# Kernel tuning notes

Hardware: AMD Instinct MI355X
Metric: run time of the kernel (lower is better)

The kernel has to match this reference:

```python
import jax, jax.numpy as jnp
import numpy as np
import math

B, N, T, D, H, NOUT = 32, 20, 100, 4, 128, 16
E = N * (N - 1)
EPS = 1e-5

def _conv1d(x, w, b):
    # x: [M, Cin, L], w: [Cout, Cin, K] -> [M, Cout, L-K+1] (VALID, stride 1)
    y = jax.lax.conv_general_dilated(x, w, (1,), 'VALID', dimension_numbers=('NCH', 'OIH', 'NCH'))
    return y + b[None, :, None]

def _bn(x, g, b, axes, caxis):
    # training-mode batch norm (biased variance), eps as in torch
    m = jnp.mean(x, axis=axes, keepdims=True)
    v = jnp.var(x, axis=axes, keepdims=True)
    sh = [1] * x.ndim
    sh[caxis] = -1
    return (x - m) / jnp.sqrt(v + EPS) * g.reshape(sh) + b.reshape(sh)

def _mlp(x, w1, b1, w2, b2, g, bb):
    h = jax.nn.elu(x @ w1.T + b1)
    h = jax.nn.elu(h @ w2.T + b2)
    return _bn(h, g, bb, (0, 1), 2)  # BN over B*E samples per feature

def _forward(rel_rec, rel_send, inputs, conv1_w, conv1_b, bn1_g, bn1_b, conv2_w, conv2_b, bn2_g, bn2_b, pred_w, pred_b, att_w, att_b, mlp1_w1, mlp1_b1, mlp1_w2, mlp1_b2, mlp1_g, mlp1_bb, mlp2_w1, mlp2_b1, mlp2_w2, mlp2_b2, mlp2_g, mlp2_bb, mlp3_w1, mlp3_b1, mlp3_w2, mlp3_b2, mlp3_g, mlp3_bb, fc_out_w, fc_out_b):
    Bv, Nv, Tv, Dv = inputs.shape
    Ev = Nv * (Nv - 1)
    # node2edge_temporal: gather sender/receiver trajectories -> [B*E, 2D, T]
    xf = inputs.reshape(Bv, Nv, Tv * Dv)
    recv = jnp.einsum('en,bnf->bef', rel_rec, xf).reshape(Bv * Ev, Tv, Dv).transpose(0, 2, 1)
    send = jnp.einsum('en,bnf->bef', rel_send, xf).reshape(Bv * Ev, Tv, Dv).transpose(0, 2, 1)
    edges = jnp.concatenate([send, recv], axis=1)
    # CNN over time
    h = jax.nn.relu(_conv1d(edges, conv1_w, conv1_b))
    h = _bn(h, bn1_g, bn1_b, (0, 2), 1)
    L = h.shape[-1] // 2
    h = h[:, :, : 2 * L].reshape(h.shape[0], h.shape[1], L, 2).max(axis=-1)  # maxpool k=2 s=2
    h = jax.nn.relu(_conv1d(h, conv2_w, conv2_b))
    h = _bn(h, bn2_g, bn2_b, (0, 2), 1)
    pred = jnp.einsum('bct,oc->bot', h, pred_w[:, :, 0]) + pred_b[None, :, None]
    att = jax.nn.softmax(jnp.einsum('bct,oc->bot', h, att_w[:, :, 0]) + att_b[None, :, None], axis=-1)
    x = (pred * att).mean(axis=-1).reshape(Bv, Ev, -1)  # attention-weighted mean pool
    x = _mlp(x, mlp1_w1, mlp1_b1, mlp1_w2, mlp1_b2, mlp1_g, mlp1_bb)
    x_skip = x
    # edge2node: scatter-mean into receivers (divide by N)
    xn = jnp.einsum('en,beh->bnh', rel_rec, x) / Nv
    xn = _mlp(xn, mlp2_w1, mlp2_b1, mlp2_w2, mlp2_b2, mlp2_g, mlp2_bb)
    # node2edge: gather back to edges
    es = jnp.einsum('en,bnh->beh', rel_send, xn)
    er = jnp.einsum('en,bnh->beh', rel_rec, xn)
    x = jnp.concatenate([es, er, x_skip], axis=2)
    x = _mlp(x, mlp3_w1, mlp3_b1, mlp3_w2, mlp3_b2, mlp3_g, mlp3_bb)
    return x @ fc_out_w.T + fc_out_b

def setup_inputs() -> dict:
    key = jax.random.key(0)
    ks = iter(jax.random.split(key, 64))
    def rn(shape, scale):
        return jax.random.normal(next(ks), shape, dtype=jnp.float32) * scale
    def xav(fo, fi):
        return rn((fo, fi), math.sqrt(2.0 / (fo + fi)))
    inputs = rn((B, N, T, D), 1.0)
    pairs = np.array([(i, j) for i in range(N) for j in range(N) if i != j])
    eye = np.eye(N, dtype=np.float32)
    d = {'inputs': inputs,
         'rel_rec': jnp.asarray(eye[pairs[:, 0]]),
         'rel_send': jnp.asarray(eye[pairs[:, 1]])}
    d['conv1_w'] = rn((H, 2 * D, 5), math.sqrt(2.0 / (5 * H)))
    d['conv1_b'] = jnp.full((H,), 0.1, jnp.float32)
    d['bn1_g'] = jnp.ones((H,), jnp.float32); d['bn1_b'] = jnp.zeros((H,), jnp.float32)
    d['conv2_w'] = rn((H, H, 5), math.sqrt(2.0 / (5 * H)))
    d['conv2_b'] = jnp.full((H,), 0.1, jnp.float32)
    d['bn2_g'] = jnp.ones((H,), jnp.float32); d['bn2_b'] = jnp.zeros((H,), jnp.float32)
    d['pred_w'] = rn((H, H, 1), math.sqrt(2.0 / H))
    d['pred_b'] = jnp.full((H,), 0.1, jnp.float32)
    d['att_w'] = rn((1, H, 1), math.sqrt(2.0))
    d['att_b'] = jnp.full((1,), 0.1, jnp.float32)
    for nm, fi in (('mlp1', H), ('mlp2', H), ('mlp3', 3 * H)):
        d[nm + '_w1'] = xav(H, fi); d[nm + '_b1'] = jnp.full((H,), 0.1, jnp.float32)
        d[nm + '_w2'] = xav(H, H); d[nm + '_b2'] = jnp.full((H,), 0.1, jnp.float32)
        d[nm + '_g'] = jnp.ones((H,), jnp.float32); d[nm + '_bb'] = jnp.zeros((H,), jnp.float32)
    d['fc_out_w'] = xav(NOUT, H)
    d['fc_out_b'] = jnp.full((NOUT,), 0.1, jnp.float32)
    return d

def reference(inputs, rel_rec, rel_send, conv1_w, conv1_b, bn1_g, bn1_b, conv2_w, conv2_b, bn2_g, bn2_b, pred_w, pred_b, att_w, att_b, mlp1_w1, mlp1_b1, mlp1_w2, mlp1_b2, mlp1_g, mlp1_bb, mlp2_w1, mlp2_b1, mlp2_w2, mlp2_b2, mlp2_g, mlp2_bb, mlp3_w1, mlp3_b1, mlp3_w2, mlp3_b2, mlp3_g, mlp3_bb, fc_out_w, fc_out_b):
    return _forward(rel_rec, rel_send, inputs, conv1_w, conv1_b, bn1_g, bn1_b, conv2_w, conv2_b, bn2_g, bn2_b, pred_w, pred_b, att_w, att_b, mlp1_w1, mlp1_b1, mlp1_w2, mlp1_b2, mlp1_g, mlp1_bb, mlp2_w1, mlp2_b1, mlp2_w2, mlp2_b2, mlp2_g, mlp2_bb, mlp3_w1, mlp3_b1, mlp3_w2, mlp3_b2, mlp3_g, mlp3_bb, fc_out_w, fc_out_b)
```

## Files before the change

kernel.cpp:

```cpp
#include <hip/hip_runtime.h>
#include <hip/hip_bf16.h>
#include <hip/hip_fp16.h>

#define BB 32
#define NN 20
#define TT 100
#define DD 4
#define HH 128
#define EE 380
#define BE 12160
#define L1 96
#define LP 48
#define L2 44
#define NOUT 16
#define EPS 1e-5f
#define NREP 64

typedef _Float16 f16x8 __attribute__((ext_vector_type(8)));
typedef _Float16 f16x4 __attribute__((ext_vector_type(4)));
typedef _Float16 f16x2 __attribute__((ext_vector_type(2)));
typedef float f32x4 __attribute__((ext_vector_type(4)));

#define S_BIAS2 0
#define S_BN1_SC 256
#define S_BN2_SC 768
#define S_M1_SC 1280
#define S_M2_SC 1792
#define S_M3_SC 2304

#define OFF_STATS 0ULL
#define OFF_SIDX 16384ULL
#define OFF_RIDX 18432ULL
#define OFF_INC 20480ULL
#define OFF_Y23 24576ULL
#define OFF_X 149446656ULL
#define OFF_BUFA 155672576ULL
#define OFF_BUFB 161898496ULL
#define OFF_XN 168124416ULL
#define OFF_T640 168452096ULL
#define OFF_REPM 168779776ULL
#define OFF_MP 171958272ULL
#define OFF_APACK OFF_T640
#define OFF_APACK1 (OFF_T640 + 163840ULL)
#define OFF_PWT (OFF_T640 + 180224ULL)
#define OFF_W2SUM (OFF_T640 + 245760ULL)
#define OFF_REP1 OFF_BUFA
#define OFF_REP2 (OFF_BUFA + 65536ULL)
#define MP_M1W1 0
#define MP_M1W2 16384
#define MP_M2W1 32768
#define MP_M2W2 49152
#define MP_M3W2 65536
#define MP_M3W1 81920

__device__ __forceinline__ float eluf(float v) { return v > 0.f ? v : expm1f(v); }

__global__ __launch_bounds__(256) void k_prep(const float* __restrict__ rel_rec,
                                              const float* __restrict__ rel_send,
                                              const float* __restrict__ w2,
                                              const float* __restrict__ w1,
                                              const float* __restrict__ pred_w,
                                              const float* __restrict__ m1w1,
                                              const float* __restrict__ m1w2,
                                              const float* __restrict__ m2w1,
                                              const float* __restrict__ m2w2,
                                              const float* __restrict__ m3w1,
                                              const float* __restrict__ m3w2,
                                              _Float16* __restrict__ apack,
                                              _Float16* __restrict__ apack1,
                                              float* __restrict__ pwt,
                                              float* __restrict__ w2sum,
                                              _Float16* __restrict__ mp,
                                              float* rep1, float* rep2, float* repm,
                                              int* sidx, int* ridx, int* inc) {
    int b = blockIdx.x;
    int tid = threadIdx.x;
    int l = tid & 63;
    if (b < 40) {
        int f = b * 4 + (tid >> 6);
        int m0 = f & 7, ks = f >> 3, s = ks & 3, k = ks >> 2;
        int m = m0 * 16 + (l & 15);
        int cbase = 32 * s + (l >> 4) * 8;
#pragma unroll
        for (int j = 0; j < 8; ++j)
            apack[(f * 64 + l) * 8 + j] = (_Float16)w2[m * 640 + (cbase + j) * 5 + k];
    } else if (b < 44) {
        int f = (b - 40) * 4 + (tid >> 6);
        int m0 = f & 7, s = f >> 3;
        int m = m0 * 16 + (l & 15);
        int cbase = 32 * s + (l >> 4) * 8;
#pragma unroll
        for (int j = 0; j < 8; ++j) {
            int c = cbase + j;
            int k = c >> 3, ci = c & 7;
            apack1[(f * 64 + l) * 8 + j] = (k < 5) ? (_Float16)w1[m * 40 + ci * 5 + k]
                                                   : (_Float16)0.f;
        }
    } else if (b == 44) {
        for (int i = tid; i < NREP * 256; i += 256) { rep1[i] = 0.f; rep2[i] = 0.f; repm[i] = 0.f; }
        for (int e = tid; e < EE; e += 256) {
            int s = 0, r = 0;
            for (int n = 0; n < NN; ++n) {
                if (rel_send[e * NN + n] > 0.5f) s = n;
                if (rel_rec[e * NN + n] > 0.5f) r = n;
            }
            sidx[e] = s; ridx[e] = r;
        }
        __syncthreads();
        if (tid < NN) {
            int k = 0;
            for (int e = 0; e < EE; ++e)
                if (ridx[e] == tid) inc[tid * (NN - 1) + (k++)] = e;
        }
    } else if (b < 53) {
        int idx = (b - 45) * 2048 + tid;
        for (int rep = 0; rep < 8; ++rep, idx += 256) {
            int o = idx >> 7, c = idx & 127;
            pwt[c * 128 + o] = pred_w[idx];
        }
    } else if (b < 117) {
        int idx = b - 53;
        const float* W; _Float16* dst; int K;
        if (idx < 8)       { W = m1w1; dst = mp + MP_M1W1; K = 128; }
        else if (idx < 16) { W = m1w2; dst = mp + MP_M1W2; K = 128; idx -= 8; }
        else if (idx < 24) { W = m2w1; dst = mp + MP_M2W1; K = 128; idx -= 16; }
        else if (idx < 32) { W = m2w2; dst = mp + MP_M2W2; K = 128; idx -= 24; }
        else if (idx < 40) { W = m3w2; dst = mp + MP_M3W2; K = 128; idx -= 32; }
        else               { W = m3w1; dst = mp + MP_M3W1; K = 384; idx -= 40; }
        int f = idx * 4 + (tid >> 6);
        int s = f >> 3, m0 = f & 7;
        int m = m0 * 16 + (l & 15);
        int cb = 32 * s + (l >> 4) * 8;
#pragma unroll
        for (int j = 0; j < 8; ++j)
            dst[(f * 64 + l) * 8 + j] = (_Float16)W[m * K + cb + j];
    } else {
        int idx = (b - 117) * 2048 + tid;
        for (int rep = 0; rep < 8; ++rep, idx += 256) {
            const float* wr = w2 + idx * 5;
            w2sum[idx] = wr[0] + wr[1] + wr[2] + wr[3] + wr[4];
        }
    }
}

__global__ __launch_bounds__(256) void k_conv1_stats(const float* __restrict__ inputs,
                                                     const _Float16* __restrict__ apack1,
                                                     const float* __restrict__ conv1_b,
                                                     const int* __restrict__ sidx,
                                                     const int* __restrict__ ridx,
                                                     float* rep1,
                                                     _Float16* __restrict__ y2p) {
    __shared__ __align__(16) _Float16 s_edgesT[104 * 8];
    __shared__ __align__(16) _Float16 s_y2t[48 * 136];
    int be = blockIdx.x;
    int b = be / EE, e = be - b * EE;
    int sn = sidx[e], rn = ridx[e];
    float* rep = rep1 + (be & (NREP - 1)) * 256;
    for (int i = threadIdx.x; i < 200; i += 256) {
        int side = (i >= 100) ? 1 : 0;
        int t = i - side * 100;
        int n = side ? rn : sn;
        float4 v = *(const float4*)(inputs + ((long long)(b * NN + n) * TT + t) * DD);
        f16x4 o = {(_Float16)v.x, (_Float16)v.y, (_Float16)v.z, (_Float16)v.w};
        *(f16x4*)(&s_edgesT[t * 8 + side * 4]) = o;
    }
    if (threadIdx.x < 32) s_edgesT[800 + threadIdx.x] = (_Float16)0.f;
    __syncthreads();
    int w = threadIdx.x >> 6, lane = threadIdx.x & 63;
    int quad = lane >> 4, l15 = lane & 15;
    f32x4 acc1[2][6];
#pragma unroll
    for (int m = 0; m < 2; ++m)
#pragma unroll
        for (int nt = 0; nt < 6; ++nt) acc1[m][nt] = (f32x4){0.f, 0.f, 0.f, 0.f};
    {
        const f16x8* Ap = (const f16x8*)apack1;
#pragma unroll
        for (int s = 0; s < 2; ++s) {
            f16x8 a0 = Ap[(s * 8 + 2 * w) * 64 + lane];
            f16x8 a1 = Ap[(s * 8 + 2 * w + 1) * 64 + lane];
#pragma unroll
            for (int nt = 0; nt < 6; ++nt) {
                f16x8 bfr = *(const f16x8*)(&s_edgesT[(nt * 16 + l15 + 4 * s + quad) * 8]);
                acc1[0][nt] = __builtin_amdgcn_mfma_f32_16x16x32_f16(a0, bfr, acc1[0][nt], 0, 0, 0);
                acc1[1][nt] = __builtin_amdgcn_mfma_f32_16x16x32_f16(a1, bfr, acc1[1][nt], 0, 0, 0);
            }
        }
    }
#pragma unroll
    for (int m = 0; m < 2; ++m) {
        int co0 = (2 * w + m) * 16 + quad * 4;
        float ss[4] = {0.f, 0.f, 0.f, 0.f}, qq[4] = {0.f, 0.f, 0.f, 0.f};
#pragma unroll
        for (int nt = 0; nt < 6; ++nt) {
            int t = nt * 16 + l15;
#pragma unroll
            for (int r = 0; r < 4; ++r) {
                float v = fmaxf(acc1[m][nt][r] + conv1_b[co0 + r], 0.f);
                ss[r] += v; qq[r] += v * v;
                float p = __shfl_xor(v, 1);
                if ((l15 & 1) == 0)
                    s_y2t[(t >> 1) * 136 + co0 + r] = (_Float16)fmaxf(v, p);
            }
        }
#pragma unroll
        for (int r = 0; r < 4; ++r) {
            float s = ss[r], q = qq[r];
            s += __shfl_xor(s, 1); s += __shfl_xor(s, 2); s += __shfl_xor(s, 4); s += __shfl_xor(s, 8);
            q += __shfl_xor(q, 1); q += __shfl_xor(q, 2); q += __shfl_xor(q, 4); q += __shfl_xor(q, 8);
            if (l15 == 0) {
                atomicAdd(&rep[co0 + r], s);
                atomicAdd(&rep[128 + co0 + r], q);
            }
        }
    }
    __syncthreads();
    _Float16* dst = y2p + (long long)be * 6144;
    for (int chunk = threadIdx.x; chunk < 768; chunk += 256) {
        int row = chunk >> 4, off = (chunk & 15) * 8;
        *(f16x8*)(dst + row * 128 + off) = *(const f16x8*)(&s_y2t[row * 136 + off]);
    }
}

__global__ void k_finalize_rep(float* __restrict__ rep, float* stats, int scIdx,
                               const float* __restrict__ g, const float* __restrict__ bb,
                               float inv_count) {
    int j = threadIdx.x;
    float s = 0.f, q = 0.f;
    for (int i = 0; i < NREP; ++i) {
        s += rep[i * 256 + j];
        q += rep[i * 256 + 128 + j];
    }
    for (int i = 0; i < NREP; ++i) {
        rep[i * 256 + j] = 0.f;
        rep[i * 256 + 128 + j] = 0.f;
    }
    float m = s * inv_count;
    float v = fmaxf(q * inv_count - m * m, 0.f);
    float sc = g[j] * rsqrtf(v + EPS);
    stats[scIdx + j] = sc;
    stats[scIdx + 128 + j] = bb[j] - m * sc;
}

__global__ void k_finalize_bn1(float* __restrict__ rep, float* stats,
                               const float* __restrict__ g, const float* __restrict__ bb,
                               const float* __restrict__ w2sum, const float* __restrict__ conv2_b,
                               float inv_count) {
    __shared__ float s_sh[128];
    int j = threadIdx.x;
    float s = 0.f, q = 0.f;
    for (int i = 0; i < NREP; ++i) {
        s += rep[i * 256 + j];
        q += rep[i * 256 + 128 + j];
    }
    for (int i = 0; i < NREP; ++i) {
        rep[i * 256 + j] = 0.f;
        rep[i * 256 + 128 + j] = 0.f;
    }
    float m = s * inv_count;
    float v = fmaxf(q * inv_count - m * m, 0.f);
    float sc = g[j] * rsqrtf(v + EPS);
    float sh = bb[j] - m * sc;
    stats[S_BN1_SC + j] = sc;
    stats[S_BN1_SC + 128 + j] = sh;
    s_sh[j] = sh;
    __syncthreads();
    float acc = conv2_b[j];
    for (int ci = 0; ci < 128; ++ci)
        acc = fmaf(w2sum[j * 128 + ci], s_sh[ci], acc);
    stats[S_BIAS2 + j] = acc;
}

__global__ __launch_bounds__(256) void k_scale(_Float16* __restrict__ apack,
                                               const float* __restrict__ stats) {
    int tid = threadIdx.x, l = tid & 63;
    int f = blockIdx.x * 4 + (tid >> 6);
    int s = (f >> 3) & 3;
    int cbase = 32 * s + (l >> 4) * 8;
    _Float16* p = apack + (f * 64 + l) * 8;
#pragma unroll
    for (int j = 0; j < 8; ++j)
        p[j] = (_Float16)((float)p[j] * stats[S_BN1_SC + cbase + j]);
}

__global__ __launch_bounds__(256) void k_conv2(_Float16* __restrict__ y23,
                                               const _Float16* __restrict__ apack,
                                               const float* __restrict__ stats,
                                               float* rep2) {
    __shared__ __align__(16) _Float16 s_y2t[2][52 * 136];
    int tid = threadIdx.x;
    int be0 = blockIdx.x * 2;
    for (int i = tid; i < 544; i += 256) {
        int ed = i / 272, rem = i - ed * 272;
        ((int*)(&s_y2t[ed][48 * 136]))[rem] = 0;
    }
    for (int i = tid; i < 1536; i += 256) {
        int ed = i / 768, rem = i - ed * 768;
        int row = rem >> 4, c0 = (rem & 15) * 8;
        *(f16x8*)(&s_y2t[ed][row * 136 + c0]) =
            *(const f16x8*)(y23 + (long long)(be0 + ed) * 6144 + rem * 8);
    }
    __syncthreads();
    int w = tid >> 6, lane = tid & 63;
    int quad = lane >> 4, l15 = lane & 15;
    int g = w & 1, e = w >> 1;
    f32x4 acc[4][3];
#pragma unroll
    for (int m = 0; m < 4; ++m)
#pragma unroll
        for (int nt = 0; nt < 3; ++nt) acc[m][nt] = (f32x4){0.f, 0.f, 0.f, 0.f};
    const f16x8* Ap = (const f16x8*)apack;
    const char* base = (const char*)&s_y2t[e][0];
#pragma unroll
    for (int k = 0; k < 5; ++k) {
#pragma unroll
        for (int s = 0; s < 4; ++s) {
            f16x8 am[4];
#pragma unroll
            for (int m = 0; m < 4; ++m)
                am[m] = Ap[((k * 4 + s) * 8 + g * 4 + m) * 64 + lane];
#pragma unroll
            for (int nt = 0; nt < 3; ++nt) {
                f16x8 bfr = *(const f16x8*)(base + (nt * 16 + l15 + k) * 272 + 64 * s + quad * 16);
#pragma unroll
                for (int m = 0; m < 4; ++m)
                    acc[m][nt] = __builtin_amdgcn_mfma_f32_16x16x32_f16(am[m], bfr, acc[m][nt], 0, 0, 0);
            }
        }
    }
    int be = be0 + e;
    _Float16* y3 = y23 + (long long)be * 6144;
    float* rep = rep2 + (be & (NREP - 1)) * 256;
#pragma unroll
    for (int m = 0; m < 4; ++m) {
        int co0 = (g * 4 + m) * 16 + quad * 4;
        float4 bs = *(const float4*)(stats + S_BIAS2 + co0);
        float ssum[4] = {0.f, 0.f, 0.f, 0.f}, qsum[4] = {0.f, 0.f, 0.f, 0.f};
#pragma unroll
        for (int nt = 0; nt < 3; ++nt) {
            int t = nt * 16 + l15;
            if (t < 44) {
                float v0 = fmaxf(acc[m][nt][0] + bs.x, 0.f);
                float v1 = fmaxf(acc[m][nt][1] + bs.y, 0.f);
                float v2 = fmaxf(acc[m][nt][2] + bs.z, 0.f);
                float v3 = fmaxf(acc[m][nt][3] + bs.w, 0.f);
                f16x4 o = {(_Float16)v0, (_Float16)v1, (_Float16)v2, (_Float16)v3};
                *(f16x4*)(y3 + t * 128 + co0) = o;
                ssum[0] += v0; qsum[0] += v0 * v0;
                ssum[1] += v1; qsum[1] += v1 * v1;
                ssum[2] += v2; qsum[2] += v2 * v2;
                ssum[3] += v3; qsum[3] += v3 * v3;
            }
        }
#pragma unroll
        for (int r = 0; r < 4; ++r) {
            float s = ssum[r], q = qsum[r];
            s += __shfl_xor(s, 1); s += __shfl_xor(s, 2); s += __shfl_xor(s, 4); s += __shfl_xor(s, 8);
            q += __shfl_xor(q, 1); q += __shfl_xor(q, 2); q += __shfl_xor(q, 4); q += __shfl_xor(q, 8);
            if (l15 == 0) {
                atomicAdd(&rep[co0 + r], s);
                atomicAdd(&rep[128 + co0 + r], q);
            }
        }
    }
}

__global__ __launch_bounds__(256) void k_predatt(const _Float16* __restrict__ y23,
                                                 const float* __restrict__ stats,
                                                 const float* __restrict__ att_w,
                                                 const float* __restrict__ att_b,
                                                 const float* __restrict__ pwt,
                                                 const float* __restrict__ pred_b,
                                                 float* __restrict__ x) {
    __shared__ float h[44 * 132];
    __shared__ float s_att[48];
    __shared__ float s_p1[256];
    __shared__ float s_p2[256];
    __shared__ float s_sc[128], s_sh[128];
    int be = blockIdx.x, tid = threadIdx.x;
    if (tid < 128) {
        s_sc[tid] = stats[S_BN2_SC + tid];
        s_sh[tid] = stats[S_BN2_SC + 128 + tid];
    }
    __syncthreads();
    const _Float16* yp = y23 + (long long)be * 6144;
    for (int i = tid; i < 704; i += 256) {
        int t = i >> 4, c0 = (i & 15) * 8;
        f16x8 v = *(const f16x8*)(yp + i * 8);
        float4 a, bq;
        a.x = fmaf((float)v[0], s_sc[c0 + 0], s_sh[c0 + 0]);
        a.y = fmaf((float)v[1], s_sc[c0 + 1], s_sh[c0 + 1]);
        a.z = fmaf((float)v[2], s_sc[c0 + 2], s_sh[c0 + 2]);
        a.w = fmaf((float)v[3], s_sc[c0 + 3], s_sh[c0 + 3]);
        bq.x = fmaf((float)v[4], s_sc[c0 + 4], s_sh[c0 + 4]);
        bq.y = fmaf((float)v[5], s_sc[c0 + 5], s_sh[c0 + 5]);
        bq.z = fmaf((float)v[6], s_sc[c0 + 6], s_sh[c0 + 6]);
        bq.w = fmaf((float)v[7], s_sc[c0 + 7], s_sh[c0 + 7]);
        *(float4*)(&h[t * 132 + c0]) = a;
        *(float4*)(&h[t * 132 + c0 + 4]) = bq;
    }
    __syncthreads();
    int w = tid >> 6, lane = tid & 63;
    {
        float aw0 = att_w[lane], aw1 = att_w[64 + lane];
        for (int tt = 0; tt < 11; ++tt) {
            int t = w * 11 + tt;
            float p = h[t * 132 + lane] * aw0 + h[t * 132 + 64 + lane] * aw1;
            p += __shfl_xor(p, 1); p += __shfl_xor(p, 2); p += __shfl_xor(p, 4);
            p += __shfl_xor(p, 8); p += __shfl_xor(p, 16); p += __shfl_xor(p, 32);
            if (lane == 0) s_att[t] = p + att_b[0];
        }
    }
    __syncthreads();
    if (w == 0) {
        float v = (lane < 44) ? s_att[lane] : -1e30f;
        float m = v;
        m = fmaxf(m, __shfl_xor(m, 1)); m = fmaxf(m, __shfl_xor(m, 2));
        m = fmaxf(m, __shfl_xor(m, 4)); m = fmaxf(m, __shfl_xor(m, 8));
        m = fmaxf(m, __shfl_xor(m, 16)); m = fmaxf(m, __shfl_xor(m, 32));
        float ev = (lane < 44) ? expf(v - m) : 0.f;
        float ss = ev;
        ss += __shfl_xor(ss, 1); ss += __shfl_xor(ss, 2); ss += __shfl_xor(ss, 4);
        ss += __shfl_xor(ss, 8); ss += __shfl_xor(ss, 16); ss += __shfl_xor(ss, 32);
        if (lane < 44) s_att[lane] = ev / ss;
    }
    __syncthreads();
    {
        int c = tid & 127, hh = tid >> 7;
        float a = 0.f;
        for (int t = hh * 22; t < hh * 22 + 22; ++t) a = fmaf(h[t * 132 + c], s_att[t], a);
        s_p1[tid] = a;
    }
    __syncthreads();
    {
        int o = tid & 127, hh = tid >> 7;
        float a = 0.f;
        for (int c = hh * 64; c < hh * 64 + 64; ++c) {
            float hw = s_p1[c] + s_p1[128 + c];
            a = fmaf(pwt[c * 128 + o], hw, a);
        }
        s_p2[tid] = a;
    }
    __syncthreads();
    if (tid < 128) {
        float a = s_p2[tid] + s_p2[128 + tid] + pred_b[tid];
        x[(long long)be * 128 + tid] = a * (1.0f / 44.0f);
    }
}

__global__ __launch_bounds__(256) void k_mlp2x(const float* __restrict__ in,
                                               const _Float16* __restrict__ wp1,
                                               const float* __restrict__ b1,
                                               const _Float16* __restrict__ wp2,
                                               const float* __restrict__ b2,
                                               float* __restrict__ out,
                                               float* __restrict__ repm) {
    __shared__ __align__(16) _Float16 s_in[64 * 136];
    __shared__ __align__(16) _Float16 s_mid[64 * 136];
    int tid = threadIdx.x;
    long long r0 = (long long)blockIdx.x * 64;
    {
        const float4* src = (const float4*)(in + r0 * 128);
        for (int i = tid; i < 2048; i += 256) {
            int row = i >> 5, c0 = (i & 31) * 4;
            float4 v = src[i];
            f16x4 o = {(_Float16)v.x, (_Float16)v.y, (_Float16)v.z, (_Float16)v.w};
            *(f16x4*)(&s_in[row * 136 + c0]) = o;
        }
    }
    __syncthreads();
    int w = tid >> 6, lane = tid & 63, quad = lane >> 4, l15 = lane & 15;
    {
        f32x4 acc[2][4];
#pragma unroll
        for (int m = 0; m < 2; ++m)
#pragma unroll
            for (int nt = 0; nt < 4; ++nt) acc[m][nt] = (f32x4){0.f, 0.f, 0.f, 0.f};
        const f16x8* Ap = (const f16x8*)wp1;
#pragma unroll
        for (int s = 0; s < 4; ++s) {
            f16x8 a0 = Ap[(s * 8 + 2 * w) * 64 + lane];
            f16x8 a1 = Ap[(s * 8 + 2 * w + 1) * 64 + lane];
#pragma unroll
            for (int nt = 0; nt < 4; ++nt) {
                f16x8 bfr = *(const f16x8*)((const char*)s_in + (nt * 16 + l15) * 272 + 64 * s + quad * 16);
                acc[0][nt] = __builtin_amdgcn_mfma_f32_16x16x32_f16(a0, bfr, acc[0][nt], 0, 0, 0);
                acc[1][nt] = __builtin_amdgcn_mfma_f32_16x16x32_f16(a1, bfr, acc[1][nt], 0, 0, 0);
            }
        }
#pragma unroll
        for (int m = 0; m < 2; ++m) {
            int j0 = (2 * w + m) * 16 + quad * 4;
            float4 bs = *(const float4*)(b1 + j0);
#pragma unroll
            for (int nt = 0; nt < 4; ++nt) {
                int row = nt * 16 + l15;
                f16x4 o = {(_Float16)eluf(acc[m][nt][0] + bs.x),
                           (_Float16)eluf(acc[m][nt][1] + bs.y),
                           (_Float16)eluf(acc[m][nt][2] + bs.z),
                           (_Float16)eluf(acc[m][nt][3] + bs.w)};
                *(f16x4*)(&s_mid[row * 136 + j0]) = o;
            }
        }
    }
    __syncthreads();
    {
        f32x4 acc[2][4];
#pragma unroll
        for (int m = 0; m < 2; ++m)
#pragma unroll
            for (int nt = 0; nt < 4; ++nt) acc[m][nt] = (f32x4){0.f, 0.f, 0.f, 0.f};
        const f16x8* Ap = (const f16x8*)wp2;
#pragma unroll
        for (int s = 0; s < 4; ++s) {
            f16x8 a0 = Ap[(s * 8 + 2 * w) * 64 + lane];
            f16x8 a1 = Ap[(s * 8 + 2 * w + 1) * 64 + lane];
#pragma unroll
            for (int nt = 0; nt < 4; ++nt) {
                f16x8 bfr = *(const f16x8*)((const char*)s_mid + (nt * 16 + l15) * 272 + 64 * s + quad * 16);
                acc[0][nt] = __builtin_amdgcn_mfma_f32_16x16x32_f16(a0, bfr, acc[0][nt], 0, 0, 0);
                acc[1][nt] = __builtin_amdgcn_mfma_f32_16x16x32_f16(a1, bfr, acc[1][nt], 0, 0, 0);
            }
        }
#pragma unroll
        for (int m = 0; m < 2; ++m) {
            int j0 = (2 * w + m) * 16 + quad * 4;
            float4 bs = *(const float4*)(b2 + j0);
            float ss[4] = {0.f, 0.f, 0.f, 0.f}, qq[4] = {0.f, 0.f, 0.f, 0.f};
#pragma unroll
            for (int nt = 0; nt < 4; ++nt) {
                int row = nt * 16 + l15;
                float v0 = eluf(acc[m][nt][0] + bs.x);
                float v1 = eluf(acc[m][nt][1] + bs.y);
                float v2 = eluf(acc[m][nt][2] + bs.z);
                float v3 = eluf(acc[m][nt][3] + bs.w);
                float4 o = {v0, v1, v2, v3};
                *(float4*)(out + (r0 + row) * 128 + j0) = o;
                ss[0] += v0; qq[0] += v0 * v0;
                ss[1] += v1; qq[1] += v1 * v1;
                ss[2] += v2; qq[2] += v2 * v2;
                ss[3] += v3; qq[3] += v3 * v3;
            }
            float* rep = repm + (blockIdx.x & (NREP - 1)) * 256;
#pragma unroll
            for (int r = 0; r < 4; ++r) {
                float s = ss[r], q = qq[r];
                s += __shfl_xor(s, 1); s += __shfl_xor(s, 2); s += __shfl_xor(s, 4); s += __shfl_xor(s, 8);
                q += __shfl_xor(q, 1); q += __shfl_xor(q, 2); q += __shfl_xor(q, 4); q += __shfl_xor(q, 8);
                if (l15 == 0) {
                    atomicAdd(&rep[j0 + r], s);
                    atomicAdd(&rep[128 + j0 + r], q);
                }
            }
        }
    }
}

__global__ __launch_bounds__(256) void k_mlp3x(const float* __restrict__ xn,
                                               const float* __restrict__ bufB,
                                               const int* __restrict__ sidx,
                                               const int* __restrict__ ridx,
                                               const float* __restrict__ stats,
                                               const _Float16* __restrict__ wp1,
                                               const float* __restrict__ b1,
                                               const _Float16* __restrict__ wp2,
                                               const float* __restrict__ b2,
                                               float* __restrict__ out,
                                               float* __restrict__ repm) {
    __shared__ __align__(16) _Float16 s_b[64 * 392];
    __shared__ __align__(16) _Float16 s_mid[64 * 136];
    __shared__ float s_st[4][128];
    __shared__ int s_s[64], s_r[64];
    int tid = threadIdx.x;
    long long r0 = (long long)blockIdx.x * 64;
    if (tid < 128) {
        s_st[0][tid] = stats[S_M2_SC + tid];
        s_st[1][tid] = stats[S_M2_SC + 128 + tid];
        s_st[2][tid] = stats[S_M1_SC + tid];
        s_st[3][tid] = stats[S_M1_SC + 128 + tid];
    }
    if (tid < 64) {
        int r = (int)r0 + tid, b = r / EE, ed = r - b * EE;
        s_s[tid] = (b * NN + sidx[ed]) * 128;
        s_r[tid] = (b * NN + ridx[ed]) * 128;
    }
    __syncthreads();
    for (int i = tid; i < 8192; i += 256) {
        int row = i >> 7, j = i & 127;
        float sc2 = s_st[0][j], sh2 = s_st[1][j];
        s_b[row * 392 + j] = (_Float16)fmaf(xn[s_s[row] + j], sc2, sh2);
        s_b[row * 392 + 128 + j] = (_Float16)fmaf(xn[s_r[row] + j], sc2, sh2);
        s_b[row * 392 + 256 + j] = (_Float16)fmaf(bufB[(r0 + row) * 128 + j], s_st[2][j], s_st[3][j]);
    }
    __syncthreads();
    int w = tid >> 6, lane = tid & 63, quad = lane >> 4, l15 = lane & 15;
    {
        f32x4 acc[2][4];
#pragma unroll
        for (int m = 0; m < 2; ++m)
#pragma unroll
            for (int nt = 0; nt < 4; ++nt) acc[m][nt] = (f32x4){0.f, 0.f, 0.f, 0.f};
        const f16x8* Ap = (const f16x8*)wp1;
#pragma unroll
        for (int s = 0; s < 12; ++s) {
            f16x8 a0 = Ap[(s * 8 + 2 * w) * 64 + lane];
            f16x8 a1 = Ap[(s * 8 + 2 * w + 1) * 64 + lane];
#pragma unroll
            for (int nt = 0; nt < 4; ++nt) {
                f16x8 bfr = *(const f16x8*)((const char*)s_b + (nt * 16 + l15) * 784 + 64 * s + quad * 16);
                acc[0][nt] = __builtin_amdgcn_mfma_f32_16x16x32_f16(a0, bfr, acc[0][nt], 0, 0, 0);
                acc[1][nt] = __builtin_amdgcn_mfma_f32_16x16x32_f16(a1, bfr, acc[1][nt], 0, 0, 0);
            }
        }
#pragma unroll
        for (int m = 0; m < 2; ++m) {
            int j0 = (2 * w + m) * 16 + quad * 4;
            float4 bs = *(const float4*)(b1 + j0);
#pragma unroll
            for (int nt = 0; nt < 4; ++nt) {
                int row = nt * 16 + l15;
                f16x4 o = {(_Float16)eluf(acc[m][nt][0] + bs.x),
                           (_Float16)eluf(acc[m][nt][1] + bs.y),
                           (_Float16)eluf(acc[m][nt][2] + bs.z),
                           (_Float16)eluf(acc[m][nt][3] + bs.w)};
                *(f16x4*)(&s_mid[row * 136 + j0]) = o;
            }
        }
    }
    __syncthreads();
    {
        f32x4 acc[2][4];
#pragma unroll
        for (int m = 0; m < 2; ++m)
#pragma unroll
            for (int nt = 0; nt < 4; ++nt) acc[m][nt] = (f32x4){0.f, 0.f, 0.f, 0.f};
        const f16x8* Ap = (const f16x8*)wp2;
#pragma unroll
        for (int s = 0; s < 4; ++s) {
            f16x8 a0 = Ap[(s * 8 + 2 * w) * 64 + lane];
            f16x8 a1 = Ap[(s * 8 + 2 * w + 1) * 64 + lane];
#pragma unroll
            for (int nt = 0; nt < 4; ++nt) {
                f16x8 bfr = *(const f16x8*)((const char*)s_mid + (nt * 16 + l15) * 272 + 64 * s + quad * 16);
                acc[0][nt] = __builtin_amdgcn_mfma_f32_16x16x32_f16(a0, bfr, acc[0][nt], 0, 0, 0);
                acc[1][nt] = __builtin_amdgcn_mfma_f32_16x16x32_f16(a1, bfr, acc[1][nt], 0, 0, 0);
            }
        }
#pragma unroll
        for (int m = 0; m < 2; ++m) {
            int j0 = (2 * w + m) * 16 + quad * 4;
            float4 bs = *(const float4*)(b2 + j0);
            float ss[4] = {0.f, 0.f, 0.f, 0.f}, qq[4] = {0.f, 0.f, 0.f, 0.f};
#pragma unroll
            for (int nt = 0; nt < 4; ++nt) {
                int row = nt * 16 + l15;
                float v0 = eluf(acc[m][nt][0] + bs.x);
                float v1 = eluf(acc[m][nt][1] + bs.y);
                float v2 = eluf(acc[m][nt][2] + bs.z);
                float v3 = eluf(acc[m][nt][3] + bs.w);
                float4 o = {v0, v1, v2, v3};
                *(float4*)(out + (r0 + row) * 128 + j0) = o;
                ss[0] += v0; qq[0] += v0 * v0;
                ss[1] += v1; qq[1] += v1 * v1;
                ss[2] += v2; qq[2] += v2 * v2;
                ss[3] += v3; qq[3] += v3 * v3;
            }
            float* rep = repm + (blockIdx.x & (NREP - 1)) * 256;
#pragma unroll
            for (int r = 0; r < 4; ++r) {
                float s = ss[r], q = qq[r];
                s += __shfl_xor(s, 1); s += __shfl_xor(s, 2); s += __shfl_xor(s, 4); s += __shfl_xor(s, 8);
                q += __shfl_xor(q, 1); q += __shfl_xor(q, 2); q += __shfl_xor(q, 4); q += __shfl_xor(q, 8);
                if (l15 == 0) {
                    atomicAdd(&rep[j0 + r], s);
                    atomicAdd(&rep[128 + j0 + r], q);
                }
            }
        }
    }
}

__global__ __launch_bounds__(128) void k_e2n(const float* __restrict__ bufB,
                                             const int* __restrict__ inc,
                                             const float* __restrict__ stats,
                                             float* __restrict__ xn) {
    int bn = blockIdx.x;
    int b = bn / NN, n = bn - b * NN;
    int j = threadIdx.x;
    float sc = stats[S_M1_SC + j], sh = stats[S_M1_SC + 128 + j];
    float s = 0.f;
    for (int k = 0; k < NN - 1; ++k) {
        int e = inc[n * (NN - 1) + k];
        s += bufB[(long long)(b * EE + e) * 128 + j];
    }
    xn[bn * 128 + j] = (s * sc + (float)(NN - 1) * sh) * (1.0f / (float)NN);
}

__global__ __launch_bounds__(256) void k_fcout(const float* __restrict__ h2,
                                               const float* __restrict__ stats,
                                               const float* __restrict__ fcw,
                                               const float* __restrict__ fcb,
                                               float* __restrict__ out) {
    __shared__ float s_x[16 * 129];
    __shared__ float s_w[16 * 129];
    int r0 = blockIdx.x * 16;
    int tid = threadIdx.x;
    for (int i = tid; i < 16 * 128; i += 256) {
        int rr = i >> 7, j = i & 127;
        s_x[rr * 129 + j] = fmaf(h2[(long long)(r0 + rr) * 128 + j],
                                 stats[S_M3_SC + j], stats[S_M3_SC + 128 + j]);
    }
    for (int i = tid; i < 16 * 128; i += 256) {
        int o = i >> 7, j = i & 127;
        s_w[o * 129 + j] = fcw[i];
    }
    __syncthreads();
    int rl = tid >> 4, o = tid & 15;
    float a = fcb[o];
    for (int j = 0; j < 128; ++j) a = fmaf(s_x[rl * 129 + j], s_w[o * 129 + j], a);
    out[(long long)(r0 + rl) * 16 + o] = a;
}

extern "C" void kernel_launch(void* const* d_in, const int* in_sizes, int n_in,
                              void* d_out, int out_size, void* d_ws, size_t ws_size,
                              hipStream_t stream) {
    const float* inputs = (const float*)d_in[0];
    const float* rel_rec = (const float*)d_in[1];
    const float* rel_send = (const float*)d_in[2];
    const float* conv1_w = (const float*)d_in[3];
    const float* conv1_b = (const float*)d_in[4];
    const float* bn1_g = (const float*)d_in[5];
    const float* bn1_b = (const float*)d_in[6];
    const float* conv2_w = (const float*)d_in[7];
    const float* conv2_b = (const float*)d_in[8];
    const float* bn2_g = (const float*)d_in[9];
    const float* bn2_b = (const float*)d_in[10];
    const float* pred_w = (const float*)d_in[11];
    const float* pred_b = (const float*)d_in[12];
    const float* att_w = (const float*)d_in[13];
    const float* att_b = (const float*)d_in[14];
    const float* m1w1 = (const float*)d_in[15];
    const float* m1b1 = (const float*)d_in[16];
    const float* m1w2 = (const float*)d_in[17];
    const float* m1b2 = (const float*)d_in[18];
    const float* m1g = (const float*)d_in[19];
    const float* m1bb = (const float*)d_in[20];
    const float* m2w1 = (const float*)d_in[21];
    const float* m2b1 = (const float*)d_in[22];
    const float* m2w2 = (const float*)d_in[23];
    const float* m2b2 = (const float*)d_in[24];
    const float* m2g = (const float*)d_in[25];
    const float* m2bb = (const float*)d_in[26];
    const float* m3w1 = (const float*)d_in[27];
    const float* m3b1 = (const float*)d_in[28];
    const float* m3w2 = (const float*)d_in[29];
    const float* m3b2 = (const float*)d_in[30];
    const float* m3g = (const float*)d_in[31];
    const float* m3bb = (const float*)d_in[32];
    const float* fcw = (const float*)d_in[33];
    const float* fcb = (const float*)d_in[34];

    char* ws = (char*)d_ws;
    float* stats = (float*)(ws + OFF_STATS);
    int* sidx = (int*)(ws + OFF_SIDX);
    int* ridx = (int*)(ws + OFF_RIDX);
    int* inc = (int*)(ws + OFF_INC);
    _Float16* y23 = (_Float16*)(ws + OFF_Y23);
    float* x = (float*)(ws + OFF_X);
    float* bufB = (float*)(ws + OFF_BUFB);
    float* xn = (float*)(ws + OFF_XN);
    _Float16* apack = (_Float16*)(ws + OFF_APACK);
    _Float16* apack1 = (_Float16*)(ws + OFF_APACK1);
    float* pwt = (float*)(ws + OFF_PWT);
    float* w2sum = (float*)(ws + OFF_W2SUM);
    float* rep1 = (float*)(ws + OFF_REP1);
    float* rep2 = (float*)(ws + OFF_REP2);
    float* repm = (float*)(ws + OFF_REPM);
    _Float16* mp = (_Float16*)(ws + OFF_MP);
    float* outp = (float*)d_out;

    hipLaunchKernelGGL(k_prep, dim3(125), dim3(256), 0, stream,
                       rel_rec, rel_send, conv2_w, conv1_w, pred_w,
                       m1w1, m1w2, m2w1, m2w2, m3w1, m3w2,
                       apack, apack1, pwt, w2sum, mp, rep1, rep2, repm, sidx, ridx, inc);
    hipLaunchKernelGGL(k_conv1_stats, dim3(BE), dim3(256), 0, stream,
                       inputs, apack1, conv1_b, sidx, ridx, rep1, y23);
    hipLaunchKernelGGL(k_finalize_bn1, dim3(1), dim3(128), 0, stream,
                       rep1, stats, bn1_g, bn1_b, w2sum, conv2_b, 1.0f / (float)(BE * L1));
    hipLaunchKernelGGL(k_scale, dim3(40), dim3(256), 0, stream, apack, stats);
    hipLaunchKernelGGL(k_conv2, dim3(BE / 2), dim3(256), 0, stream,
                       y23, apack, stats, rep2);
    hipLaunchKernelGGL(k_finalize_rep, dim3(1), dim3(128), 0, stream,
                       rep2, stats, S_BN2_SC, bn2_g, bn2_b, 1.0f / (float)(BE * L2));
    hipLaunchKernelGGL(k_predatt, dim3(BE), dim3(256), 0, stream,
                       y23, stats, att_w, att_b, pwt, pred_b, x);
    hipLaunchKernelGGL(k_mlp2x, dim3(BE / 64), dim3(256), 0, stream,
                       x, mp + MP_M1W1, m1b1, mp + MP_M1W2, m1b2, bufB, repm);
    hipLaunchKernelGGL(k_finalize_rep, dim3(1), dim3(128), 0, stream,
                       repm, stats, S_M1_SC, m1g, m1bb, 1.0f / (float)BE);
    hipLaunchKernelGGL(k_e2n, dim3(BB * NN), dim3(128), 0, stream, bufB, inc, stats, xn);
    hipLaunchKernelGGL(k_mlp2x, dim3(BB * NN / 64), dim3(256), 0, stream,
                       xn, mp + MP_M2W1, m2b1, mp + MP_M2W2, m2b2, xn, repm);
    hipLaunchKernelGGL(k_finalize_rep, dim3(1), dim3(128), 0, stream,
                       repm, stats, S_M2_SC, m2g, m2bb, 1.0f / (float)(BB * NN));
    hipLaunchKernelGGL(k_mlp3x, dim3(BE / 64), dim3(256), 0, stream,
                       xn, bufB, sidx, ridx, stats, mp + MP_M3W1, m3b1, mp + MP_M3W2, m3b2,
                       bufB, repm);
    hipLaunchKernelGGL(k_finalize_rep, dim3(1), dim3(128), 0, stream,
                       repm, stats, S_M3_SC, m3g, m3bb, 1.0f / (float)BE);
    hipLaunchKernelGGL(k_fcout, dim3(BE / 16), dim3(256), 0, stream, bufB, stats, fcw, fcb, outp);
    (void)in_sizes; (void)n_in; (void)out_size; (void)ws_size;
}
```

Measured before the change: 585.2 us.

## Fold MLP batch-norm finalize into consumer kernels and trim conv2 shared padding

```diff
diff --git a/kernel.cpp b/kernel.cpp
--- a/kernel.cpp
+++ b/kernel.cpp
@@ -24,9 +24,6 @@
 #define S_BIAS2 0
 #define S_BN1_SC 256
 #define S_BN2_SC 768
-#define S_M1_SC 1280
-#define S_M2_SC 1792
-#define S_M3_SC 2304
 
 #define OFF_STATS 0ULL
 #define OFF_SIDX 16384ULL
@@ -97,7 +94,8 @@
                                                    : (_Float16)0.f;
         }
     } else if (b == 44) {
-        for (int i = tid; i < NREP * 256; i += 256) { rep1[i] = 0.f; rep2[i] = 0.f; repm[i] = 0.f; }
+        for (int i = tid; i < NREP * 256; i += 256) { rep1[i] = 0.f; rep2[i] = 0.f; }
+        for (int i = tid; i < 3 * NREP * 256; i += 256) repm[i] = 0.f;
         for (int e = tid; e < EE; e += 256) {
             int s = 0, r = 0;
             for (int n = 0; n < NN; ++n) {
@@ -287,13 +285,9 @@
                                                const _Float16* __restrict__ apack,
                                                const float* __restrict__ stats,
                                                float* rep2) {
-    __shared__ __align__(16) _Float16 s_y2t[2][52 * 136];
+    __shared__ __align__(16) _Float16 s_y2t[2][48 * 136];
     int tid = threadIdx.x;
     int be0 = blockIdx.x * 2;
-    for (int i = tid; i < 544; i += 256) {
-        int ed = i / 272, rem = i - ed * 272;
-        ((int*)(&s_y2t[ed][48 * 136]))[rem] = 0;
-    }
     for (int i = tid; i < 1536; i += 256) {
         int ed = i / 768, rem = i - ed * 768;
         int row = rem >> 4, c0 = (rem & 15) * 8;
@@ -321,7 +315,9 @@
                 am[m] = Ap[((k * 4 + s) * 8 + g * 4 + m) * 64 + lane];
 #pragma unroll
             for (int nt = 0; nt < 3; ++nt) {
-                f16x8 bfr = *(const f16x8*)(base + (nt * 16 + l15 + k) * 272 + 64 * s + quad * 16);
+                int r = nt * 16 + l15 + k;
+                if (nt == 2) r = (r > 47) ? 47 : r;
+                f16x8 bfr = *(const f16x8*)(base + r * 272 + 64 * s + quad * 16);
 #pragma unroll
                 for (int m = 0; m < 4; ++m)
                     acc[m][nt] = __builtin_amdgcn_mfma_f32_16x16x32_f16(am[m], bfr, acc[m][nt], 0, 0, 0);
@@ -560,13 +556,18 @@
                                                const float* __restrict__ bufB,
                                                const int* __restrict__ sidx,
                                                const int* __restrict__ ridx,
-                                               const float* __restrict__ stats,
+                                               const float* __restrict__ repm1,
+                                               const float* __restrict__ repm2,
+                                               const float* __restrict__ m1g,
+                                               const float* __restrict__ m1bb,
+                                               const float* __restrict__ m2g,
+                                               const float* __restrict__ m2bb,
                                                const _Float16* __restrict__ wp1,
                                                const float* __restrict__ b1,
                                                const _Float16* __restrict__ wp2,
                                                const float* __restrict__ b2,
                                                float* __restrict__ out,
-                                               float* __restrict__ repm) {
+                                               float* __restrict__ repm3) {
     __shared__ __align__(16) _Float16 s_b[64 * 392];
     __shared__ __align__(16) _Float16 s_mid[64 * 136];
     __shared__ float s_st[4][128];
@@ -574,10 +575,26 @@
     int tid = threadIdx.x;
     long long r0 = (long long)blockIdx.x * 64;
     if (tid < 128) {
-        s_st[0][tid] = stats[S_M2_SC + tid];
-        s_st[1][tid] = stats[S_M2_SC + 128 + tid];
-        s_st[2][tid] = stats[S_M1_SC + tid];
-        s_st[3][tid] = stats[S_M1_SC + 128 + tid];
+        float s = 0.f, q = 0.f;
+        for (int i = 0; i < NREP; ++i) {
+            s += repm2[i * 256 + tid];
+            q += repm2[i * 256 + 128 + tid];
+        }
+        float mm = s * (1.0f / (float)(BB * NN));
+        float vv = fmaxf(q * (1.0f / (float)(BB * NN)) - mm * mm, 0.f);
+        float sc = m2g[tid] * rsqrtf(vv + EPS);
+        s_st[0][tid] = sc;
+        s_st[1][tid] = m2bb[tid] - mm * sc;
+        s = 0.f; q = 0.f;
+        for (int i = 0; i < NREP; ++i) {
+            s += repm1[i * 256 + tid];
+            q += repm1[i * 256 + 128 + tid];
+        }
+        mm = s * (1.0f / (float)BE);
+        vv = fmaxf(q * (1.0f / (float)BE) - mm * mm, 0.f);
+        sc = m1g[tid] * rsqrtf(vv + EPS);
+        s_st[2][tid] = sc;
+        s_st[3][tid] = m1bb[tid] - mm * sc;
     }
     if (tid < 64) {
         int r = (int)r0 + tid, b = r / EE, ed = r - b * EE;
@@ -665,7 +682,7 @@
                 ss[2] += v2; qq[2] += v2 * v2;
                 ss[3] += v3; qq[3] += v3 * v3;
             }
-            float* rep = repm + (blockIdx.x & (NREP - 1)) * 256;
+            float* rep = repm3 + (blockIdx.x & (NREP - 1)) * 256;
 #pragma unroll
             for (int r = 0; r < 4; ++r) {
                 float s = ss[r], q = qq[r];
@@ -682,12 +699,22 @@
 
 __global__ __launch_bounds__(128) void k_e2n(const float* __restrict__ bufB,
                                              const int* __restrict__ inc,
-                                             const float* __restrict__ stats,
+                                             const float* __restrict__ repm1,
+                                             const float* __restrict__ m1g,
+                                             const float* __restrict__ m1bb,
                                              float* __restrict__ xn) {
     int bn = blockIdx.x;
     int b = bn / NN, n = bn - b * NN;
     int j = threadIdx.x;
-    float sc = stats[S_M1_SC + j], sh = stats[S_M1_SC + 128 + j];
+    float s0 = 0.f, q0 = 0.f;
+    for (int i = 0; i < NREP; ++i) {
+        s0 += repm1[i * 256 + j];
+        q0 += repm1[i * 256 + 128 + j];
+    }
+    float mm = s0 * (1.0f / (float)BE);
+    float vv = fmaxf(q0 * (1.0f / (float)BE) - mm * mm, 0.f);
+    float sc = m1g[j] * rsqrtf(vv + EPS);
+    float sh = m1bb[j] - mm * sc;
     float s = 0.f;
     for (int k = 0; k < NN - 1; ++k) {
         int e = inc[n * (NN - 1) + k];
@@ -697,18 +724,33 @@
 }
 
 __global__ __launch_bounds__(256) void k_fcout(const float* __restrict__ h2,
-                                               const float* __restrict__ stats,
+                                               const float* __restrict__ repm3,
+                                               const float* __restrict__ m3g,
+                                               const float* __restrict__ m3bb,
                                                const float* __restrict__ fcw,
                                                const float* __restrict__ fcb,
                                                float* __restrict__ out) {
     __shared__ float s_x[16 * 129];
     __shared__ float s_w[16 * 129];
+    __shared__ float s_sc[128], s_sh[128];
     int r0 = blockIdx.x * 16;
     int tid = threadIdx.x;
+    if (tid < 128) {
+        float s = 0.f, q = 0.f;
+        for (int i = 0; i < NREP; ++i) {
+            s += repm3[i * 256 + tid];
+            q += repm3[i * 256 + 128 + tid];
+        }
+        float mm = s * (1.0f / (float)BE);
+        float vv = fmaxf(q * (1.0f / (float)BE) - mm * mm, 0.f);
+        float sc = m3g[tid] * rsqrtf(vv + EPS);
+        s_sc[tid] = sc;
+        s_sh[tid] = m3bb[tid] - mm * sc;
+    }
+    __syncthreads();
     for (int i = tid; i < 16 * 128; i += 256) {
         int rr = i >> 7, j = i & 127;
-        s_x[rr * 129 + j] = fmaf(h2[(long long)(r0 + rr) * 128 + j],
-                                 stats[S_M3_SC + j], stats[S_M3_SC + 128 + j]);
+        s_x[rr * 129 + j] = fmaf(h2[(long long)(r0 + rr) * 128 + j], s_sc[j], s_sh[j]);
     }
     for (int i = tid; i < 16 * 128; i += 256) {
         int o = i >> 7, j = i & 127;
@@ -775,14 +817,16 @@
     float* w2sum = (float*)(ws + OFF_W2SUM);
     float* rep1 = (float*)(ws + OFF_REP1);
     float* rep2 = (float*)(ws + OFF_REP2);
-    float* repm = (float*)(ws + OFF_REPM);
+    float* repm1 = (float*)(ws + OFF_REPM);
+    float* repm2 = (float*)(ws + OFF_REPM + 65536ULL);
+    float* repm3 = (float*)(ws + OFF_REPM + 131072ULL);
     _Float16* mp = (_Float16*)(ws + OFF_MP);
     float* outp = (float*)d_out;
 
     hipLaunchKernelGGL(k_prep, dim3(125), dim3(256), 0, stream,
                        rel_rec, rel_send, conv2_w, conv1_w, pred_w,
                        m1w1, m1w2, m2w1, m2w2, m3w1, m3w2,
-                       apack, apack1, pwt, w2sum, mp, rep1, rep2, repm, sidx, ridx, inc);
+                       apack, apack1, pwt, w2sum, mp, rep1, rep2, repm1, sidx, ridx, inc);
     hipLaunchKernelGGL(k_conv1_stats, dim3(BE), dim3(256), 0, stream,
                        inputs, apack1, conv1_b, sidx, ridx, rep1, y23);
     hipLaunchKernelGGL(k_finalize_bn1, dim3(1), dim3(128), 0, stream,
@@ -795,19 +839,14 @@
     hipLaunchKernelGGL(k_predatt, dim3(BE), dim3(256), 0, stream,
                        y23, stats, att_w, att_b, pwt, pred_b, x);
     hipLaunchKernelGGL(k_mlp2x, dim3(BE / 64), dim3(256), 0, stream,
-                       x, mp + MP_M1W1, m1b1, mp + MP_M1W2, m1b2, bufB, repm);
-    hipLaunchKernelGGL(k_finalize_rep, dim3(1), dim3(128), 0, stream,
-                       repm, stats, S_M1_SC, m1g, m1bb, 1.0f / (float)BE);
-    hipLaunchKernelGGL(k_e2n, dim3(BB * NN), dim3(128), 0, stream, bufB, inc, stats, xn);
+                       x, mp + MP_M1W1, m1b1, mp + MP_M1W2, m1b2, bufB, repm1);
+    hipLaunchKernelGGL(k_e2n, dim3(BB * NN), dim3(128), 0, stream, bufB, inc, repm1, m1g, m1bb, xn);
     hipLaunchKernelGGL(k_mlp2x, dim3(BB * NN / 64), dim3(256), 0, stream,
-                       xn, mp + MP_M2W1, m2b1, mp + MP_M2W2, m2b2, xn, repm);
-    hipLaunchKernelGGL(k_finalize_rep, dim3(1), dim3(128), 0, stream,
-                       repm, stats, S_M2_SC, m2g, m2bb, 1.0f / (float)(BB * NN));
+                       xn, mp + MP_M2W1, m2b1, mp + MP_M2W2, m2b2, xn, repm2);
     hipLaunchKernelGGL(k_mlp3x, dim3(BE / 64), dim3(256), 0, stream,
-                       xn, bufB, sidx, ridx, stats, mp + MP_M3W1, m3b1, mp + MP_M3W2, m3b2,
-                       bufB, repm);
-    hipLaunchKernelGGL(k_finalize_rep, dim3(1), dim3(128), 0, stream,
-                       repm, stats, S_M3_SC, m3g, m3bb, 1.0f / (float)BE);
-    hipLaunchKernelGGL(k_fcout, dim3(BE / 16), dim3(256), 0, stream, bufB, stats, fcw, fcb, outp);
+                       xn, bufB, sidx, ridx, repm1, repm2, m1g, m1bb, m2g, m2bb,
+                       mp + MP_M3W1, m3b1, mp + MP_M3W2, m3b2, bufB, repm3);
+    hipLaunchKernelGGL(k_fcout, dim3(BE / 16), dim3(256), 0, stream,
+                       bufB, repm3, m3g, m3bb, fcw, fcb, outp);
     (void)in_sizes; (void)n_in; (void)out_size; (void)ws_size;
 }
```

After: 587.0 us, median of 2. About the same (+0.3%).
